# Optimization experiments

Measured on AMD Instinct MI355X. Metric: run time of the kernel, lower is better.

## Reference

```python
import jax, jax.numpy as jnp
import numpy as np

CLAMP_LO, CLAMP_HI, CLAMP_GATE_MAX = -10.0, 10.0, 10.0
E, TOPK = 8, 2
M, K, N = 2048, 2048, 1408  # tokens, hidden_dim, intermediate_dim
CAPACITY = 2 * (M * TOPK // E)


def setup_inputs() -> dict:
    key = jax.random.key(0)
    ks = jax.random.split(key, 6)
    bk = 1.0 / np.sqrt(K)  # kaiming_uniform(a=sqrt(5)) bound = 1/sqrt(fan_in)
    bn = 1.0 / np.sqrt(N)
    return {
        "flat_h": jax.random.normal(ks[0], (M, K), jnp.float32),
        "flat_idx": jax.random.randint(ks[1], (M, TOPK), 0, E),
        "flat_gate": jax.random.uniform(ks[2], (M, TOPK), jnp.float32),
        "gate_weight": jax.random.uniform(ks[3], (E, N, K), jnp.float32, -bk, bk),
        "up_weight": jax.random.uniform(ks[4], (E, N, K), jnp.float32, -bk, bk),
        "down_weight": jax.random.uniform(ks[5], (E, K, N), jnp.float32, -bn, bn),
    }


def reference(flat_h, flat_idx, flat_gate, gate_weight, up_weight, down_weight):
    m, top_k = flat_idx.shape
    k = flat_h.shape[1]
    e = gate_weight.shape[0]
    r = m * top_k

    expert_id = flat_idx.reshape(-1)                                   # (R,)
    gate = flat_gate.reshape(-1)                                       # (R,)
    token_index = jnp.repeat(jnp.arange(m, dtype=jnp.int32), top_k)    # (R,)

    # stable sort rows by expert id (mirrors torch.argsort(..., stable=True))
    sort_idx = jnp.argsort(expert_id, stable=True)
    sorted_eid = expert_id[sort_idx]
    tok_sorted = token_index[sort_idx]
    gate_sorted = gate[sort_idx]

    # position of each sorted row inside its expert group
    counts = jnp.bincount(expert_id, length=e)
    starts = jnp.concatenate([jnp.zeros(1, counts.dtype), jnp.cumsum(counts)[:-1]])
    pos = jnp.arange(r) - starts[sorted_eid]                           # (R,)

    # dispatch: scatter sorted tokens into fixed-capacity (E, C, K) buffer
    buf = jnp.zeros((e, CAPACITY, k), flat_h.dtype)
    buf = buf.at[sorted_eid, pos].set(flat_h[tok_sorted])

    # grouped GEMMs: weights stored (E, out, in) like nn.Linear
    g = jnp.einsum("eck,enk->ecn", buf, gate_weight)
    g = jnp.minimum(g, CLAMP_GATE_MAX)
    u = jnp.clip(jnp.einsum("eck,enk->ecn", buf, up_weight), CLAMP_LO, CLAMP_HI)
    h = jax.nn.silu(g) * u                                             # SwiGLU (E, C, N)
    d = jnp.einsum("ecn,ekn->eck", h, down_weight)                     # (E, C, K)

    # combine: gather each routed row back, weight by gate, sum over top_k slots
    expert_out = d[sorted_eid, pos]                                    # (R, K)
    weighted = expert_out * gate_sorted[:, None]
    out = jnp.zeros((m, k), flat_h.dtype).at[tok_sorted].add(weighted)
    return out
```

## Files before the change

### kernel.cpp

```cpp
#include <hip/hip_runtime.h>

#define M_TOK 2048
#define KDIM 2048
#define NDIM 1408
#define NEXP 8
#define RROWS (M_TOK * 2)
#define CAP 1024

typedef __attribute__((ext_vector_type(8))) short short8;
typedef __attribute__((ext_vector_type(4))) float f32x4;

__device__ __forceinline__ unsigned short bf16rn(float f) {
    unsigned int u = __builtin_bit_cast(unsigned int, f);
    u += 0x7FFFu + ((u >> 16) & 1u);
    return (unsigned short)(u >> 16);
}
__device__ __forceinline__ unsigned int pk2(float a, float b) {
    return (unsigned int)bf16rn(a) | ((unsigned int)bf16rn(b) << 16);
}

__device__ __forceinline__ void glds16(const void* g, void* l) {
    __builtin_amdgcn_global_load_lds(
        (const __attribute__((address_space(1))) unsigned int*)g,
        (__attribute__((address_space(3))) unsigned int*)l, 16, 0, 0);
}

__global__ void k_route(const float* __restrict__ h, const int* __restrict__ idx,
                        const float* __restrict__ gate, int* __restrict__ cnt,
                        int* __restrict__ tok_of, float* __restrict__ gate_of,
                        unsigned short* __restrict__ bufA) {
    int r = blockIdx.x;
    __shared__ int s_ep;
    if (threadIdx.x == 0) {
        int e = idx[r];
        int p = atomicAdd(&cnt[e], 1);
        tok_of[e * CAP + p] = r >> 1;
        gate_of[e * CAP + p] = gate[r];
        s_ep = e * CAP + p;
    }
    __syncthreads();
    int ep = s_ep;
    const float4* src = (const float4*)(h + (size_t)(r >> 1) * KDIM) + threadIdx.x * 2;
    float4 a = src[0], b = src[1];
    uint4 o;
    o.x = pk2(a.x, a.y); o.y = pk2(a.z, a.w);
    o.z = pk2(b.x, b.y); o.w = pk2(b.z, b.w);
    *((uint4*)(bufA + (size_t)ep * KDIM) + threadIdx.x) = o;
}

__global__ void k_cvt(const float* __restrict__ src, unsigned short* __restrict__ dst) {
    int i = blockIdx.x * blockDim.x + threadIdx.x;
    const float4* s = (const float4*)src + (size_t)i * 2;
    float4 a = s[0], b = s[1];
    uint4 o;
    o.x = pk2(a.x, a.y); o.y = pk2(a.z, a.w);
    o.z = pk2(b.x, b.y); o.w = pk2(b.z, b.w);
    ((uint4*)dst)[i] = o;
}

__global__ __launch_bounds__(256, 2)
void k_gemm1(const unsigned short* __restrict__ bufA,
             const unsigned short* __restrict__ gwb,
             const unsigned short* __restrict__ uwb,
             const int* __restrict__ cnt, unsigned short* __restrict__ hbuf) {
    const int e = blockIdx.z;
    const int m0 = blockIdx.y * 128;
    if (m0 >= cnt[e]) return;
    const int n0 = blockIdx.x * 128;

    const unsigned short* A = bufA + (size_t)e * CAP * KDIM;
    const unsigned short* G = gwb + (size_t)e * NDIM * KDIM;
    const unsigned short* U = uwb + (size_t)e * NDIM * KDIM;

    __shared__ unsigned short sA[128 * 32];
    __shared__ unsigned short sG[128 * 32];
    __shared__ unsigned short sU[128 * 32];

    const int tid = threadIdx.x;
    const int lane = tid & 63;
    const int wave = tid >> 6;
    const int wm = (wave >> 1) * 64, wn = (wave & 1) * 64;
    const int q = lane >> 4, l15 = lane & 15;
    const int r4 = lane >> 2, c8 = (lane & 3) * 8;
    const int seg0 = wave * 2;

    f32x4 accG[4][4] = {};
    f32x4 accU[4][4] = {};

    for (int k0 = 0; k0 < KDIM; k0 += 32) {
        __syncthreads();
#pragma unroll
        for (int c = 0; c < 2; c++) {
            int seg = seg0 + c;
            int row = seg * 16 + r4;
            glds16(A + (size_t)(m0 + row) * KDIM + k0 + c8, &sA[seg * 512]);
            glds16(G + (size_t)(n0 + row) * KDIM + k0 + c8, &sG[seg * 512]);
            glds16(U + (size_t)(n0 + row) * KDIM + k0 + c8, &sU[seg * 512]);
        }
        __syncthreads();

        short8 af[4], gf[4], uf[4];
#pragma unroll
        for (int i = 0; i < 4; i++) {
            af[i] = *(const short8*)&sA[(wm + i * 16 + l15) * 32 + q * 8];
            gf[i] = *(const short8*)&sG[(wn + i * 16 + l15) * 32 + q * 8];
            uf[i] = *(const short8*)&sU[(wn + i * 16 + l15) * 32 + q * 8];
        }
#pragma unroll
        for (int i = 0; i < 4; i++)
#pragma unroll
            for (int j = 0; j < 4; j++) {
                accG[i][j] = __builtin_amdgcn_mfma_f32_16x16x32_bf16(af[i], gf[j], accG[i][j], 0, 0, 0);
                accU[i][j] = __builtin_amdgcn_mfma_f32_16x16x32_bf16(af[i], uf[j], accU[i][j], 0, 0, 0);
            }
    }

    unsigned short* H = hbuf + (size_t)e * CAP * NDIM;
#pragma unroll
    for (int i = 0; i < 4; i++)
#pragma unroll
        for (int j = 0; j < 4; j++) {
            int col = n0 + wn + j * 16 + l15;
#pragma unroll
            for (int rg = 0; rg < 4; rg++) {
                int row = m0 + wm + i * 16 + q * 4 + rg;
                float g = accG[i][j][rg];
                float u = accU[i][j][rg];
                g = fminf(g, 10.f);
                u = fminf(fmaxf(u, -10.f), 10.f);
                float hv = g / (1.f + __expf(-g)) * u;
                H[(size_t)row * NDIM + col] = bf16rn(hv);
            }
        }
}

__global__ __launch_bounds__(256, 2)
void k_gemm2(const unsigned short* __restrict__ hbuf,
             const unsigned short* __restrict__ dwb, const int* __restrict__ cnt,
             const int* __restrict__ tok_of, const float* __restrict__ gate_of,
             float* __restrict__ out) {
    const int e = blockIdx.z;
    const int cnt_e = cnt[e];
    const int m0 = blockIdx.y * 128;
    if (m0 >= cnt_e) return;
    const int n0 = blockIdx.x * 128;

    const unsigned short* A = hbuf + (size_t)e * CAP * NDIM;
    const unsigned short* B = dwb + (size_t)e * KDIM * NDIM;

    __shared__ unsigned short sA[128 * 32];
    __shared__ unsigned short sB[128 * 32];

    const int tid = threadIdx.x;
    const int lane = tid & 63;
    const int wave = tid >> 6;
    const int wm = (wave >> 1) * 64, wn = (wave & 1) * 64;
    const int q = lane >> 4, l15 = lane & 15;
    const int r4 = lane >> 2, c8 = (lane & 3) * 8;
    const int seg0 = wave * 2;

    f32x4 acc[4][4] = {};

    for (int k0 = 0; k0 < NDIM; k0 += 32) {
        __syncthreads();
#pragma unroll
        for (int c = 0; c < 2; c++) {
            int seg = seg0 + c;
            int row = seg * 16 + r4;
            glds16(A + (size_t)(m0 + row) * NDIM + k0 + c8, &sA[seg * 512]);
            glds16(B + (size_t)(n0 + row) * NDIM + k0 + c8, &sB[seg * 512]);
        }
        __syncthreads();

        short8 af[4], bfr[4];
#pragma unroll
        for (int i = 0; i < 4; i++) {
            af[i] = *(const short8*)&sA[(wm + i * 16 + l15) * 32 + q * 8];
            bfr[i] = *(const short8*)&sB[(wn + i * 16 + l15) * 32 + q * 8];
        }
#pragma unroll
        for (int i = 0; i < 4; i++)
#pragma unroll
            for (int j = 0; j < 4; j++)
                acc[i][j] = __builtin_amdgcn_mfma_f32_16x16x32_bf16(af[i], bfr[j], acc[i][j], 0, 0, 0);
    }

#pragma unroll
    for (int i = 0; i < 4; i++) {
#pragma unroll
        for (int rg = 0; rg < 4; rg++) {
            int row = m0 + wm + i * 16 + q * 4 + rg;
            if (row < cnt_e) {
                int tok = tok_of[e * CAP + row];
                float gt = gate_of[e * CAP + row];
                float* orow = out + (size_t)tok * KDIM + n0 + wn + l15;
#pragma unroll
                for (int j = 0; j < 4; j++)
                    atomicAdd(orow + j * 16, acc[i][j][rg] * gt);
            }
        }
    }
}

extern "C" void kernel_launch(void* const* d_in, const int* in_sizes, int n_in,
                              void* d_out, int out_size, void* d_ws, size_t ws_size,
                              hipStream_t stream) {
    const float* flat_h = (const float*)d_in[0];
    const int* flat_idx = (const int*)d_in[1];
    const float* flat_gate = (const float*)d_in[2];
    const float* gw = (const float*)d_in[3];
    const float* uw = (const float*)d_in[4];
    const float* dwn = (const float*)d_in[5];
    float* out = (float*)d_out;

    char* w = (char*)d_ws;
    int* cnt = (int*)w;
    int* tok_of = (int*)(w + 256);
    float* gate_of = (float*)(w + 256 + NEXP * CAP * 4);
    unsigned short* bufA = (unsigned short*)(w + (1ull << 20));
    unsigned short* hbuf = (unsigned short*)(w + (33ull << 20));
    unsigned short* gwb  = (unsigned short*)(w + (56ull << 20));
    unsigned short* uwb  = (unsigned short*)(w + (100ull << 20));
    unsigned short* dwb  = (unsigned short*)(w + (144ull << 20));

    hipMemsetAsync(cnt, 0, 256, stream);
    hipMemsetAsync(out, 0, (size_t)M_TOK * KDIM * 4, stream);

    const int welems8 = NEXP * NDIM * KDIM / 8;
    k_cvt<<<welems8 / 256, 256, 0, stream>>>(gw, gwb);
    k_cvt<<<welems8 / 256, 256, 0, stream>>>(uw, uwb);
    k_cvt<<<welems8 / 256, 256, 0, stream>>>(dwn, dwb);

    k_route<<<RROWS, 256, 0, stream>>>(flat_h, flat_idx, flat_gate, cnt, tok_of, gate_of, bufA);
    k_gemm1<<<dim3(NDIM / 128, CAP / 128, NEXP), 256, 0, stream>>>(bufA, gwb, uwb, cnt, hbuf);
    k_gemm2<<<dim3(KDIM / 128, CAP / 128, NEXP), 256, 0, stream>>>(hbuf, dwb, cnt, tok_of, gate_of, out);
}
```

Baseline: 518.7 us.

## Double K-tile with swizzled LDS, interleave experts, replace atomic combine with gather kernel

Both grouped GEMMs now stage 64-wide K tiles in LDS with an XOR swizzle on the column blocks to avoid bank conflicts and halve barrier count. Grid launch is flattened with expert as the fastest-varying index to balance empty blocks across CUs. The down-projection writes plain fp32 rows into a per-slot buffer (aliased over dead weight buffers), and a new combine kernel gathers the two slots per token with their gates, removing atomics and the output memset. The three weight conversions are merged into one launch. Costs include an extra 64MB intermediate write/read and more LDS per block.

```diff
diff --git a/kernel.cpp b/kernel.cpp
--- a/kernel.cpp
+++ b/kernel.cpp
@@ -26,17 +26,16 @@
 }
 
 __global__ void k_route(const float* __restrict__ h, const int* __restrict__ idx,
-                        const float* __restrict__ gate, int* __restrict__ cnt,
-                        int* __restrict__ tok_of, float* __restrict__ gate_of,
+                        int* __restrict__ cnt, int* __restrict__ slot_of,
                         unsigned short* __restrict__ bufA) {
     int r = blockIdx.x;
     __shared__ int s_ep;
     if (threadIdx.x == 0) {
         int e = idx[r];
         int p = atomicAdd(&cnt[e], 1);
-        tok_of[e * CAP + p] = r >> 1;
-        gate_of[e * CAP + p] = gate[r];
-        s_ep = e * CAP + p;
+        int ep = e * CAP + p;
+        slot_of[r] = ep;
+        s_ep = ep;
     }
     __syncthreads();
     int ep = s_ep;
@@ -48,7 +47,12 @@
     *((uint4*)(bufA + (size_t)ep * KDIM) + threadIdx.x) = o;
 }
 
-__global__ void k_cvt(const float* __restrict__ src, unsigned short* __restrict__ dst) {
+__global__ void k_cvt3(const float* __restrict__ s0, const float* __restrict__ s1,
+                       const float* __restrict__ s2,
+                       unsigned short* __restrict__ d0, unsigned short* __restrict__ d1,
+                       unsigned short* __restrict__ d2) {
+    const float* src = blockIdx.y == 0 ? s0 : (blockIdx.y == 1 ? s1 : s2);
+    unsigned short* dst = blockIdx.y == 0 ? d0 : (blockIdx.y == 1 ? d1 : d2);
     int i = blockIdx.x * blockDim.x + threadIdx.x;
     const float4* s = (const float4*)src + (size_t)i * 2;
     float4 a = s[0], b = s[1];
@@ -63,56 +67,67 @@
              const unsigned short* __restrict__ gwb,
              const unsigned short* __restrict__ uwb,
              const int* __restrict__ cnt, unsigned short* __restrict__ hbuf) {
-    const int e = blockIdx.z;
-    const int m0 = blockIdx.y * 128;
+    const int f = blockIdx.x;
+    const int e = f & 7;
+    const int t = f >> 3;
+    const int n_blk = t % 11;
+    const int m_blk = t / 11;
+    const int m0 = m_blk * 128;
     if (m0 >= cnt[e]) return;
-    const int n0 = blockIdx.x * 128;
+    const int n0 = n_blk * 128;
 
     const unsigned short* A = bufA + (size_t)e * CAP * KDIM;
     const unsigned short* G = gwb + (size_t)e * NDIM * KDIM;
     const unsigned short* U = uwb + (size_t)e * NDIM * KDIM;
 
-    __shared__ unsigned short sA[128 * 32];
-    __shared__ unsigned short sG[128 * 32];
-    __shared__ unsigned short sU[128 * 32];
+    __shared__ unsigned short sA[128 * 64];
+    __shared__ unsigned short sG[128 * 64];
+    __shared__ unsigned short sU[128 * 64];
 
     const int tid = threadIdx.x;
     const int lane = tid & 63;
     const int wave = tid >> 6;
     const int wm = (wave >> 1) * 64, wn = (wave & 1) * 64;
     const int q = lane >> 4, l15 = lane & 15;
-    const int r4 = lane >> 2, c8 = (lane & 3) * 8;
-    const int seg0 = wave * 2;
+    const int sr = lane >> 3;
+    const int scb = (lane & 7) ^ (sr & 7);
+    const int xi = l15 & 7;
+    const int cbl0 = (q ^ xi) * 8;
+    const int cbl1 = ((4 + q) ^ xi) * 8;
 
     f32x4 accG[4][4] = {};
     f32x4 accU[4][4] = {};
 
-    for (int k0 = 0; k0 < KDIM; k0 += 32) {
-        __syncthreads();
-#pragma unroll
-        for (int c = 0; c < 2; c++) {
-            int seg = seg0 + c;
-            int row = seg * 16 + r4;
-            glds16(A + (size_t)(m0 + row) * KDIM + k0 + c8, &sA[seg * 512]);
-            glds16(G + (size_t)(n0 + row) * KDIM + k0 + c8, &sG[seg * 512]);
-            glds16(U + (size_t)(n0 + row) * KDIM + k0 + c8, &sU[seg * 512]);
-        }
-        __syncthreads();
-
-        short8 af[4], gf[4], uf[4];
-#pragma unroll
-        for (int i = 0; i < 4; i++) {
-            af[i] = *(const short8*)&sA[(wm + i * 16 + l15) * 32 + q * 8];
-            gf[i] = *(const short8*)&sG[(wn + i * 16 + l15) * 32 + q * 8];
-            uf[i] = *(const short8*)&sU[(wn + i * 16 + l15) * 32 + q * 8];
-        }
-#pragma unroll
-        for (int i = 0; i < 4; i++)
-#pragma unroll
-            for (int j = 0; j < 4; j++) {
-                accG[i][j] = __builtin_amdgcn_mfma_f32_16x16x32_bf16(af[i], gf[j], accG[i][j], 0, 0, 0);
-                accU[i][j] = __builtin_amdgcn_mfma_f32_16x16x32_bf16(af[i], uf[j], accU[i][j], 0, 0, 0);
-            }
+    for (int k0 = 0; k0 < KDIM; k0 += 64) {
+        __syncthreads();
+#pragma unroll
+        for (int c = 0; c < 4; c++) {
+            int seg = wave * 4 + c;
+            int row = seg * 8 + sr;
+            glds16(A + (size_t)(m0 + row) * KDIM + k0 + scb * 8, &sA[seg * 512]);
+            glds16(G + (size_t)(n0 + row) * KDIM + k0 + scb * 8, &sG[seg * 512]);
+            glds16(U + (size_t)(n0 + row) * KDIM + k0 + scb * 8, &sU[seg * 512]);
+        }
+        __syncthreads();
+
+#pragma unroll
+        for (int kh = 0; kh < 2; kh++) {
+            const int co = kh ? cbl1 : cbl0;
+            short8 af[4], gf[4], uf[4];
+#pragma unroll
+            for (int i = 0; i < 4; i++) {
+                af[i] = *(const short8*)&sA[(wm + i * 16 + l15) * 64 + co];
+                gf[i] = *(const short8*)&sG[(wn + i * 16 + l15) * 64 + co];
+                uf[i] = *(const short8*)&sU[(wn + i * 16 + l15) * 64 + co];
+            }
+#pragma unroll
+            for (int i = 0; i < 4; i++)
+#pragma unroll
+                for (int j = 0; j < 4; j++) {
+                    accG[i][j] = __builtin_amdgcn_mfma_f32_16x16x32_bf16(af[i], gf[j], accG[i][j], 0, 0, 0);
+                    accU[i][j] = __builtin_amdgcn_mfma_f32_16x16x32_bf16(af[i], uf[j], accU[i][j], 0, 0, 0);
+                }
+        }
     }
 
     unsigned short* H = hbuf + (size_t)e * CAP * NDIM;
@@ -137,68 +152,98 @@
 __global__ __launch_bounds__(256, 2)
 void k_gemm2(const unsigned short* __restrict__ hbuf,
              const unsigned short* __restrict__ dwb, const int* __restrict__ cnt,
-             const int* __restrict__ tok_of, const float* __restrict__ gate_of,
-             float* __restrict__ out) {
-    const int e = blockIdx.z;
+             float* __restrict__ dbuf) {
+    const int f = blockIdx.x;
+    const int e = f & 7;
+    const int t = f >> 3;
+    const int n_blk = t & 15;
+    const int m_blk = t >> 4;
     const int cnt_e = cnt[e];
-    const int m0 = blockIdx.y * 128;
+    const int m0 = m_blk * 128;
     if (m0 >= cnt_e) return;
-    const int n0 = blockIdx.x * 128;
+    const int n0 = n_blk * 128;
 
     const unsigned short* A = hbuf + (size_t)e * CAP * NDIM;
     const unsigned short* B = dwb + (size_t)e * KDIM * NDIM;
 
-    __shared__ unsigned short sA[128 * 32];
-    __shared__ unsigned short sB[128 * 32];
+    __shared__ unsigned short sA[128 * 64];
+    __shared__ unsigned short sB[128 * 64];
 
     const int tid = threadIdx.x;
     const int lane = tid & 63;
     const int wave = tid >> 6;
     const int wm = (wave >> 1) * 64, wn = (wave & 1) * 64;
     const int q = lane >> 4, l15 = lane & 15;
-    const int r4 = lane >> 2, c8 = (lane & 3) * 8;
-    const int seg0 = wave * 2;
+    const int sr = lane >> 3;
+    const int scb = (lane & 7) ^ (sr & 7);
+    const int xi = l15 & 7;
+    const int cbl0 = (q ^ xi) * 8;
+    const int cbl1 = ((4 + q) ^ xi) * 8;
 
     f32x4 acc[4][4] = {};
 
-    for (int k0 = 0; k0 < NDIM; k0 += 32) {
-        __syncthreads();
-#pragma unroll
-        for (int c = 0; c < 2; c++) {
-            int seg = seg0 + c;
-            int row = seg * 16 + r4;
-            glds16(A + (size_t)(m0 + row) * NDIM + k0 + c8, &sA[seg * 512]);
-            glds16(B + (size_t)(n0 + row) * NDIM + k0 + c8, &sB[seg * 512]);
-        }
-        __syncthreads();
-
-        short8 af[4], bfr[4];
-#pragma unroll
-        for (int i = 0; i < 4; i++) {
-            af[i] = *(const short8*)&sA[(wm + i * 16 + l15) * 32 + q * 8];
-            bfr[i] = *(const short8*)&sB[(wn + i * 16 + l15) * 32 + q * 8];
-        }
-#pragma unroll
-        for (int i = 0; i < 4; i++)
-#pragma unroll
-            for (int j = 0; j < 4; j++)
-                acc[i][j] = __builtin_amdgcn_mfma_f32_16x16x32_bf16(af[i], bfr[j], acc[i][j], 0, 0, 0);
-    }
-
+    for (int k0 = 0; k0 < NDIM; k0 += 64) {
+        __syncthreads();
+#pragma unroll
+        for (int c = 0; c < 4; c++) {
+            int seg = wave * 4 + c;
+            int row = seg * 8 + sr;
+            glds16(A + (size_t)(m0 + row) * NDIM + k0 + scb * 8, &sA[seg * 512]);
+            glds16(B + (size_t)(n0 + row) * NDIM + k0 + scb * 8, &sB[seg * 512]);
+        }
+        __syncthreads();
+
+#pragma unroll
+        for (int kh = 0; kh < 2; kh++) {
+            const int co = kh ? cbl1 : cbl0;
+            short8 af[4], bfr[4];
+#pragma unroll
+            for (int i = 0; i < 4; i++) {
+                af[i] = *(const short8*)&sA[(wm + i * 16 + l15) * 64 + co];
+                bfr[i] = *(const short8*)&sB[(wn + i * 16 + l15) * 64 + co];
+            }
+#pragma unroll
+            for (int i = 0; i < 4; i++)
+#pragma unroll
+                for (int j = 0; j < 4; j++)
+                    acc[i][j] = __builtin_amdgcn_mfma_f32_16x16x32_bf16(af[i], bfr[j], acc[i][j], 0, 0, 0);
+        }
+    }
+
+    float* D = dbuf + (size_t)e * CAP * KDIM;
 #pragma unroll
     for (int i = 0; i < 4; i++) {
 #pragma unroll
         for (int rg = 0; rg < 4; rg++) {
             int row = m0 + wm + i * 16 + q * 4 + rg;
             if (row < cnt_e) {
-                int tok = tok_of[e * CAP + row];
-                float gt = gate_of[e * CAP + row];
-                float* orow = out + (size_t)tok * KDIM + n0 + wn + l15;
+                float* drow = D + (size_t)row * KDIM + n0 + wn + l15;
 #pragma unroll
                 for (int j = 0; j < 4; j++)
-                    atomicAdd(orow + j * 16, acc[i][j][rg] * gt);
-            }
-        }
+                    drow[j * 16] = acc[i][j][rg];
+            }
+        }
+    }
+}
+
+__global__ void k_combine(const float* __restrict__ dbuf, const int* __restrict__ slot_of,
+                          const float* __restrict__ gate, float* __restrict__ out) {
+    int tk = blockIdx.x;
+    int s0 = slot_of[2 * tk], s1 = slot_of[2 * tk + 1];
+    float g0 = gate[2 * tk], g1 = gate[2 * tk + 1];
+    const float4* r0 = (const float4*)(dbuf + (size_t)s0 * KDIM);
+    const float4* r1 = (const float4*)(dbuf + (size_t)s1 * KDIM);
+    float4* o = (float4*)(out + (size_t)tk * KDIM);
+    int i = threadIdx.x * 2;
+#pragma unroll
+    for (int c = 0; c < 2; c++) {
+        float4 a = r0[i + c], b = r1[i + c];
+        float4 v;
+        v.x = g0 * a.x + g1 * b.x;
+        v.y = g0 * a.y + g1 * b.y;
+        v.z = g0 * a.z + g1 * b.z;
+        v.w = g0 * a.w + g1 * b.w;
+        o[i + c] = v;
     }
 }
 
@@ -215,23 +260,20 @@
 
     char* w = (char*)d_ws;
     int* cnt = (int*)w;
-    int* tok_of = (int*)(w + 256);
-    float* gate_of = (float*)(w + 256 + NEXP * CAP * 4);
-    unsigned short* bufA = (unsigned short*)(w + (1ull << 20));
-    unsigned short* hbuf = (unsigned short*)(w + (33ull << 20));
-    unsigned short* gwb  = (unsigned short*)(w + (56ull << 20));
-    unsigned short* uwb  = (unsigned short*)(w + (100ull << 20));
-    unsigned short* dwb  = (unsigned short*)(w + (144ull << 20));
+    int* slot_of = (int*)(w + 256);
+    unsigned short* bufA = (unsigned short*)(w + 1048576ull);
+    unsigned short* hbuf = (unsigned short*)(w + 34603008ull);
+    unsigned short* gwb  = (unsigned short*)(w + 57671680ull);
+    unsigned short* uwb  = (unsigned short*)(w + 103809024ull);
+    unsigned short* dwb  = (unsigned short*)(w + 149946368ull);
+    float* dbuf = (float*)(w + 57671680ull);
 
     hipMemsetAsync(cnt, 0, 256, stream);
-    hipMemsetAsync(out, 0, (size_t)M_TOK * KDIM * 4, stream);
 
     const int welems8 = NEXP * NDIM * KDIM / 8;
-    k_cvt<<<welems8 / 256, 256, 0, stream>>>(gw, gwb);
-    k_cvt<<<welems8 / 256, 256, 0, stream>>>(uw, uwb);
-    k_cvt<<<welems8 / 256, 256, 0, stream>>>(dwn, dwb);
-
-    k_route<<<RROWS, 256, 0, stream>>>(flat_h, flat_idx, flat_gate, cnt, tok_of, gate_of, bufA);
-    k_gemm1<<<dim3(NDIM / 128, CAP / 128, NEXP), 256, 0, stream>>>(bufA, gwb, uwb, cnt, hbuf);
-    k_gemm2<<<dim3(KDIM / 128, CAP / 128, NEXP), 256, 0, stream>>>(hbuf, dwb, cnt, tok_of, gate_of, out);
-}
+    k_cvt3<<<dim3(welems8 / 256, 3), 256, 0, stream>>>(gw, uw, dwn, gwb, uwb, dwb);
+    k_route<<<RROWS, 256, 0, stream>>>(flat_h, flat_idx, cnt, slot_of, bufA);
+    k_gemm1<<<8 * 11 * 8, 256, 0, stream>>>(bufA, gwb, uwb, cnt, hbuf);
+    k_gemm2<<<8 * 16 * 8, 256, 0, stream>>>(hbuf, dwb, cnt, dbuf);
+    k_combine<<<M_TOK, 256, 0, stream>>>(dbuf, slot_of, flat_gate, out);
+}
```

Result: faster. 461.8 us (-11.0%).
